# Kernel optimization log

Measured on AMD Instinct MI355X. Metric: run time of the kernel, lower is better.

Reference implementation:

```python
import jax, jax.numpy as jnp
import numpy as np

B, C, H, W = 4, 64, 128, 128
Q = 65536
OUT_SIZE = 256  # output image side -> cell = 2/OUT_SIZE
HIDDEN = 256
D_IN = C + 2 + 2  # feat + rel_coord + rel_cell


def setup_inputs() -> dict:
    key = jax.random.key(0)
    ks = jax.random.split(key, 8)
    feat = jax.random.normal(ks[0], (B, C, H, W), dtype=jnp.float32)
    coord = jax.random.uniform(ks[1], (B, Q, 2), dtype=jnp.float32, minval=-1.0, maxval=1.0)
    cell = jnp.full((B, Q, 2), 2.0 / OUT_SIZE, dtype=jnp.float32)

    def lin(k, din, dout):
        return jax.random.normal(k, (din, dout), dtype=jnp.float32) * (1.0 / np.sqrt(din))

    w0 = lin(ks[2], D_IN, HIDDEN)
    w1 = lin(ks[3], HIDDEN, HIDDEN)
    w2 = lin(ks[4], HIDDEN, HIDDEN)
    w3 = lin(ks[5], HIDDEN, HIDDEN)
    w4 = lin(ks[6], HIDDEN, 3)
    z = lambda d: jnp.zeros((d,), dtype=jnp.float32)
    return {"feat": feat, "coord": coord, "cell": cell,
            "w0": w0, "b0": z(HIDDEN), "w1": w1, "b1": z(HIDDEN),
            "w2": w2, "b2": z(HIDDEN), "w3": w3, "b3": z(HIDDEN),
            "w4": w4, "b4": z(3)}


def _liif(feat, coord, cell, ws, bs):
    b, c, h, w = feat.shape
    eps = 1e-6
    rx, ry = 1.0 / h, 1.0 / w  # 2/h/2, 2/w/2
    # local ensemble shifts, loop order vx outer, vy inner: (-1,-1),(-1,1),(1,-1),(1,1)
    shifts = jnp.array([[-rx, -ry], [-rx, ry], [rx, -ry], [rx, ry]], dtype=feat.dtype) + eps
    feat_flat = feat.reshape(b, c, h * w)
    cell_scale = jnp.array([h, w], dtype=feat.dtype)
    rel_cell = cell * cell_scale  # same for all branches

    def branch(shift):
        cshift = jnp.clip(coord + shift, -1.0 + eps, 1.0 - eps)
        # nearest grid_sample, align_corners=False: idx = floor((x+1)*size/2), clamped
        iy = jnp.clip(jnp.floor((cshift[..., 0] + 1.0) * (h * 0.5)), 0.0, h - 1.0).astype(jnp.int32)
        ix = jnp.clip(jnp.floor((cshift[..., 1] + 1.0) * (w * 0.5)), 0.0, w - 1.0).astype(jnp.int32)
        idx = iy * w + ix  # [B, Q]
        q_feat = jnp.take_along_axis(feat_flat, idx[:, None, :], axis=2)  # [B, C, Q]
        q_feat = q_feat.transpose(0, 2, 1)  # [B, Q, C]
        # feat_coord at the gathered pixel (make_coord values)
        qc0 = -1.0 + (2.0 * iy.astype(feat.dtype) + 1.0) / h
        qc1 = -1.0 + (2.0 * ix.astype(feat.dtype) + 1.0) / w
        rel0 = (coord[..., 0] - qc0) * h
        rel1 = (coord[..., 1] - qc1) * w
        inp = jnp.concatenate([q_feat, rel0[..., None], rel1[..., None], rel_cell], axis=-1)
        x = inp
        for wi, bi in zip(ws[:-1], bs[:-1]):
            x = jax.nn.relu(x @ wi + bi)
        pred = x @ ws[-1] + bs[-1]  # [B, Q, 3]
        area = jnp.abs(rel0 * rel1) + 1e-9  # [B, Q]
        return pred, area

    preds, areas = jax.vmap(branch)(shifts)  # [4,B,Q,3], [4,B,Q]
    tot = areas.sum(axis=0)
    # diagonal weight swap: 0<->3, 1<->2  == reverse
    wgt = areas[::-1] / tot
    return (preds * wgt[..., None]).sum(axis=0)  # [B, Q, 3]


def reference(feat, coord, cell, w0, b0, w1, b1, w2, b2, w3, b3, w4, b4):
    ws = [w0, w1, w2, w3, w4]
    bs = [b0, b1, b2, b3, b4]
    return _liif(feat, coord, cell, ws, bs)
```

## Files before the change

### kernel.cpp

```cpp
#include <hip/hip_runtime.h>
#include <cstdint>

typedef __bf16 bf16x8 __attribute__((ext_vector_type(8)));
typedef float f32x4 __attribute__((ext_vector_type(4)));
typedef float f32x16 __attribute__((ext_vector_type(16)));
typedef unsigned int u32x4 __attribute__((ext_vector_type(4)));
typedef unsigned int u32x2 __attribute__((ext_vector_type(2)));
typedef unsigned short u16;
typedef unsigned int u32;

#define HH 128
#define WW 128
#define CC 64
#define QQ 65536
#define BB 4

#define RS 264

#define L0_OFF 0
#define L1_OFF 20480
#define L2_OFF 86016
#define L3_OFF 151552
#define W4_OFF 217088
#define FEATT_BYTE_OFF 524288u

__global__ void pack_weights(const float* __restrict__ w0,
                             const float* __restrict__ w1,
                             const float* __restrict__ w2,
                             const float* __restrict__ w3,
                             const float* __restrict__ w4,
                             u16* __restrict__ ws_us) {
    int bid = blockIdx.x;
    int lane = threadIdx.x;
    int dst, kbase, n, Ksrc, Ncols;
    const float* w;
    if (bid < 424) {
        int tile, off;
        if (bid < 40)       { tile = bid;       off = L0_OFF; w = w0; Ksrc = 68;  }
        else if (bid < 168) { tile = bid - 40;  off = L1_OFF; w = w1; Ksrc = 256; }
        else if (bid < 296) { tile = bid - 168; off = L2_OFF; w = w2; Ksrc = 256; }
        else                { tile = bid - 296; off = L3_OFF; w = w3; Ksrc = 256; }
        int nt = tile & 7, ks = tile >> 3;
        n = nt * 32 + (lane & 31);
        kbase = ks * 16 + (lane >> 5) * 8;
        Ncols = 256;
        dst = off + tile * 512 + lane * 8;
    } else {
        int kt = bid - 424;
        n = lane & 15;
        kbase = kt * 32 + (lane >> 4) * 8;
        w = w4; Ksrc = 256; Ncols = 3;
        dst = W4_OFF + kt * 512 + lane * 8;
    }
    unsigned int d[4];
    for (int i = 0; i < 4; ++i) {
        unsigned int lo, hi;
        {
            int k = kbase + 2 * i;
            float x = (k < Ksrc && n < Ncols) ? w[k * Ncols + n] : 0.0f;
            __bf16 hb = (__bf16)x;
            lo = (unsigned int)__builtin_bit_cast(u16, hb);
        }
        {
            int k = kbase + 2 * i + 1;
            float x = (k < Ksrc && n < Ncols) ? w[k * Ncols + n] : 0.0f;
            __bf16 hb = (__bf16)x;
            hi = (unsigned int)__builtin_bit_cast(u16, hb);
        }
        d[i] = lo | (hi << 16);
    }
    u32x4 pk = { d[0], d[1], d[2], d[3] };
    *reinterpret_cast<u32x4*>(ws_us + dst) = pk;
}

__global__ void prep_featT(const float* __restrict__ feat, u16* __restrict__ featT) {
    __shared__ u16 tile[128 * 66];
    int bid = blockIdx.x;
    int b = bid >> 7, y = bid & 127;
    for (int idx = threadIdx.x; idx < CC * WW; idx += 256) {
        int c = idx >> 7, x = idx & 127;
        float v = feat[(((b * CC + c) * HH + y) * WW) + x];
        __bf16 hb = (__bf16)v;
        tile[x * 66 + c] = __builtin_bit_cast(u16, hb);
    }
    __syncthreads();
    for (int idx = threadIdx.x; idx < 2048; idx += 256) {
        int x = idx >> 4, c4 = (idx & 15) * 4;
        const u16* src = tile + x * 66 + c4;
        u32x2 d;
        d[0] = (unsigned int)src[0] | ((unsigned int)src[1] << 16);
        d[1] = (unsigned int)src[2] | ((unsigned int)src[3] << 16);
        *reinterpret_cast<u32x2*>(featT + ((b * HH + y) * WW + x) * CC + c4) = d;
    }
}

__device__ __forceinline__ void preload6(u32x4 w[6], const u32x4* __restrict__ b,
                                         int v, int kstr) {
    w[0] = b[v];
    w[1] = b[v + 64];
    w[2] = b[v + kstr];
    w[3] = b[v + kstr + 64];
    w[4] = b[v + 2 * kstr];
    w[5] = b[v + 2 * kstr + 64];
}

template <int NKS>
__device__ __forceinline__ void gemm32(const u16* __restrict__ src,
                                       u16* __restrict__ dst,
                                       const u32x4* __restrict__ wbase,
                                       const float* __restrict__ bias,
                                       int wave, int lane,
                                       const u32x4 wpre[6],
                                       u32x4 wnxt[6],
                                       const u32x4* __restrict__ wnb,
                                       int vnxt, int nkstr) {
    f32x16 acc[2][2] = {};
    const int l31 = lane & 31;
    const int hi = lane >> 5;
    const int voff = wave * 128 + lane;
    const u16* xb = src + l31 * RS + hi * 8;
    u16* db = dst + l31 * RS + wave * 64 + hi * 4;

    u32x4 wq[3][2];
    wq[0][0] = wpre[0]; wq[0][1] = wpre[1];
    wq[1][0] = wpre[2]; wq[1][1] = wpre[3];
    wq[2][0] = wpre[4]; wq[2][1] = wpre[5];

    bf16x8 xc[2][2];
    xc[0][0] = __builtin_bit_cast(bf16x8, *reinterpret_cast<const u32x4*>(xb));
    xc[0][1] = __builtin_bit_cast(bf16x8, *reinterpret_cast<const u32x4*>(xb + 32 * RS));
    xc[1][0] = __builtin_bit_cast(bf16x8, *reinterpret_cast<const u32x4*>(xb + 16));
    xc[1][1] = __builtin_bit_cast(bf16x8, *reinterpret_cast<const u32x4*>(xb + 32 * RS + 16));

#pragma unroll
    for (int ks = 0; ks < NKS; ++ks) {
        const int ws = ks % 3;
        const int xs = ks & 1;
        acc[0][0] = __builtin_amdgcn_mfma_f32_32x32x16_bf16(
            __builtin_bit_cast(bf16x8, wq[ws][0]), xc[xs][0], acc[0][0], 0, 0, 0);
        acc[1][0] = __builtin_amdgcn_mfma_f32_32x32x16_bf16(
            __builtin_bit_cast(bf16x8, wq[ws][1]), xc[xs][0], acc[1][0], 0, 0, 0);
        if (ks + 2 < NKS)
            xc[xs][0] = __builtin_bit_cast(bf16x8,
                *reinterpret_cast<const u32x4*>(xb + (ks + 2) * 16));
        acc[0][1] = __builtin_amdgcn_mfma_f32_32x32x16_bf16(
            __builtin_bit_cast(bf16x8, wq[ws][0]), xc[xs][1], acc[0][1], 0, 0, 0);
        acc[1][1] = __builtin_amdgcn_mfma_f32_32x32x16_bf16(
            __builtin_bit_cast(bf16x8, wq[ws][1]), xc[xs][1], acc[1][1], 0, 0, 0);
        if (ks + 2 < NKS)
            xc[xs][1] = __builtin_bit_cast(bf16x8,
                *reinterpret_cast<const u32x4*>(xb + 32 * RS + (ks + 2) * 16));
        if (ks + 3 < NKS) {
            const u32x4* wn = wbase + (ks + 3) * 512;
            wq[ws][0] = wn[voff];
            wq[ws][1] = wn[voff + 64];
        }
    }

    wnxt[0] = wnb[vnxt];
    wnxt[1] = wnb[vnxt + 64];
    wnxt[2] = wnb[vnxt + nkstr];
    wnxt[3] = wnb[vnxt + nkstr + 64];
    wnxt[4] = wnb[vnxt + 2 * nkstr];
    wnxt[5] = wnb[vnxt + 2 * nkstr + 64];

#pragma unroll
    for (int ft = 0; ft < 2; ++ft) {
        const int fb = wave * 64 + ft * 32 + hi * 4;
#pragma unroll
        for (int q4 = 0; q4 < 4; ++q4) {
            f32x4 bv = *reinterpret_cast<const f32x4*>(bias + fb + q4 * 8);
#pragma unroll
            for (int st = 0; st < 2; ++st) {
                float v0 = fmaxf(acc[ft][st][q4 * 4 + 0] + bv[0], 0.0f);
                float v1 = fmaxf(acc[ft][st][q4 * 4 + 1] + bv[1], 0.0f);
                float v2 = fmaxf(acc[ft][st][q4 * 4 + 2] + bv[2], 0.0f);
                float v3 = fmaxf(acc[ft][st][q4 * 4 + 3] + bv[3], 0.0f);
                __bf16 h0 = (__bf16)v0, h1 = (__bf16)v1, h2 = (__bf16)v2, h3 = (__bf16)v3;
                u32x2 d;
                d[0] = (u32)__builtin_bit_cast(u16, h0) | ((u32)__builtin_bit_cast(u16, h1) << 16);
                d[1] = (u32)__builtin_bit_cast(u16, h2) | ((u32)__builtin_bit_cast(u16, h3) << 16);
                *reinterpret_cast<u32x2*>(db + st * 32 * RS + ft * 32 + q4 * 8) = d;
            }
        }
    }
}

__global__ __launch_bounds__(256, 2) void liif_main(
    const float* __restrict__ coord, const float* __restrict__ cell,
    const float* __restrict__ b0, const float* __restrict__ b1,
    const float* __restrict__ b2, const float* __restrict__ b3,
    const float* __restrict__ b4,
    const u16* __restrict__ wpack, const u16* __restrict__ featT,
    float* __restrict__ out) {
    __shared__ u16 bufs[2 * 64 * RS];
    __shared__ float areasLDS[64];

    u16* buf0 = bufs;
    u16* buf1 = bufs + 64 * RS;

    const int t = threadIdx.x;
    const int wave = t >> 6, lane = t & 63;
    const int row = t >> 2, p = t & 3;

    const int bq = blockIdx.x * 16 + (row >> 2);
    const int v = row & 3;
    const int b = bq >> 16;
    const float c0 = coord[bq * 2 + 0];
    const float c1 = coord[bq * 2 + 1];
    const float rc0 = cell[bq * 2 + 0] * 128.0f;
    const float rc1 = cell[bq * 2 + 1] * 128.0f;
    const float eps = 1e-6f;
    const float sx = ((v & 2) ? 0.0078125f : -0.0078125f) + eps;
    const float sy = ((v & 1) ? 0.0078125f : -0.0078125f) + eps;
    float cs0 = fminf(fmaxf(c0 + sx, -1.0f + eps), 1.0f - eps);
    float cs1 = fminf(fmaxf(c1 + sy, -1.0f + eps), 1.0f - eps);
    float fy = fminf(fmaxf(floorf((cs0 + 1.0f) * 64.0f), 0.0f), 127.0f);
    float fx = fminf(fmaxf(floorf((cs1 + 1.0f) * 64.0f), 0.0f), 127.0f);
    int iy = (int)fy, ix = (int)fx;
    float qc0 = -1.0f + (2.0f * fy + 1.0f) * 0.0078125f;
    float qc1 = -1.0f + (2.0f * fx + 1.0f) * 0.0078125f;
    float rel0 = (c0 - qc0) * 128.0f;
    float rel1 = (c1 - qc1) * 128.0f;
    float area = fabsf(rel0 * rel1) + 1e-9f;

    {
        const u16* fr = featT + (((b * HH + iy) * WW + ix) * CC) + p * 16;
        u32x4 f0 = *reinterpret_cast<const u32x4*>(fr);
        u32x4 f1 = *reinterpret_cast<const u32x4*>(fr + 8);
        u16* sb = buf0 + row * RS;
        *reinterpret_cast<u32x4*>(sb + p * 16) = f0;
        *reinterpret_cast<u32x4*>(sb + p * 16 + 8) = f1;
        u32x4 e = { 0u, 0u, 0u, 0u };
        if (p == 0) {
            __bf16 h0 = (__bf16)rel0, h1 = (__bf16)rel1, h2 = (__bf16)rc0, h3 = (__bf16)rc1;
            e[0] = (u32)__builtin_bit_cast(u16, h0) | ((u32)__builtin_bit_cast(u16, h1) << 16);
            e[1] = (u32)__builtin_bit_cast(u16, h2) | ((u32)__builtin_bit_cast(u16, h3) << 16);
            areasLDS[row] = area;
        }
        *reinterpret_cast<u32x4*>(sb + 64 + p * 8) = e;
    }

    const u32x4* wp = reinterpret_cast<const u32x4*>(wpack);
    const u32x4* wp0 = wp + (L0_OFF / 8);
    const u32x4* wp1 = wp + (L1_OFF / 8);
    const u32x4* wp2 = wp + (L2_OFF / 8);
    const u32x4* wp3 = wp + (L3_OFF / 8);
    const u32x4* wp4 = wp + (W4_OFF / 8);
    const int voff = wave * 128 + lane;

    u32x4 wA[6], wB[6];
    preload6(wA, wp0, voff, 512);
    __syncthreads();
    gemm32<5>(buf0, buf1, wp0, b0, wave, lane, wA, wB, wp1, voff, 512);
    __syncthreads();
    gemm32<16>(buf1, buf0, wp1, b1, wave, lane, wB, wA, wp2, voff, 512);
    __syncthreads();
    gemm32<16>(buf0, buf1, wp2, b2, wave, lane, wA, wB, wp3, voff, 512);
    __syncthreads();
    gemm32<16>(buf1, buf0, wp3, b3, wave, lane, wB, wA, wp4, lane, 128);
    u32x4 w4hi[2];
#pragma unroll
    for (int kt = 0; kt < 2; ++kt) w4hi[kt] = wp4[(kt + 6) * 64 + lane];
    __syncthreads();

    const int l15 = lane & 15;
    const int qd = lane >> 4;
    const u16* xb = buf0 + (wave * 16 + l15) * RS + qd * 8;
    f32x4 accf = {};
#pragma unroll
    for (int kt = 0; kt < 6; ++kt) {
        bf16x8 x = __builtin_bit_cast(bf16x8,
            *reinterpret_cast<const u32x4*>(xb + kt * 32));
        accf = __builtin_amdgcn_mfma_f32_16x16x32_bf16(
            __builtin_bit_cast(bf16x8, wA[kt]), x, accf, 0, 0, 0);
    }
#pragma unroll
    for (int kt = 6; kt < 8; ++kt) {
        bf16x8 x = __builtin_bit_cast(bf16x8,
            *reinterpret_cast<const u32x4*>(xb + kt * 32));
        accf = __builtin_amdgcn_mfma_f32_16x16x32_bf16(
            __builtin_bit_cast(bf16x8, w4hi[kt - 6]), x, accf, 0, 0, 0);
    }
    float a = areasLDS[wave * 16 + l15];
    float a1 = a + __shfl_xor(a, 1);
    float asum = a1 + __shfl_xor(a1, 2);
    float aopp = __shfl_xor(a, 3);
    float wgt = aopp / asum;
    float o0 = (accf[0] + b4[0]) * wgt;
    float o1 = (accf[1] + b4[1]) * wgt;
    float o2 = (accf[2] + b4[2]) * wgt;
    o0 += __shfl_xor(o0, 1); o0 += __shfl_xor(o0, 2);
    o1 += __shfl_xor(o1, 1); o1 += __shfl_xor(o1, 2);
    o2 += __shfl_xor(o2, 1); o2 += __shfl_xor(o2, 2);

    if (qd == 0 && (l15 & 3) == 0) {
        int obq = blockIdx.x * 16 + wave * 4 + (l15 >> 2);
        out[obq * 3 + 0] = o0;
        out[obq * 3 + 1] = o1;
        out[obq * 3 + 2] = o2;
    }
}

extern "C" void kernel_launch(void* const* d_in, const int* in_sizes, int n_in,
                              void* d_out, int out_size, void* d_ws, size_t ws_size,
                              hipStream_t stream) {
    const float* feat  = (const float*)d_in[0];
    const float* coord = (const float*)d_in[1];
    const float* cell  = (const float*)d_in[2];
    const float* w0 = (const float*)d_in[3];
    const float* b0 = (const float*)d_in[4];
    const float* w1 = (const float*)d_in[5];
    const float* b1 = (const float*)d_in[6];
    const float* w2 = (const float*)d_in[7];
    const float* b2 = (const float*)d_in[8];
    const float* w3 = (const float*)d_in[9];
    const float* b3 = (const float*)d_in[10];
    const float* w4 = (const float*)d_in[11];
    const float* b4 = (const float*)d_in[12];

    u16* ws_us = (u16*)d_ws;
    u16* featT = (u16*)((char*)d_ws + FEATT_BYTE_OFF);

    hipLaunchKernelGGL(pack_weights, dim3(432), dim3(64), 0, stream,
                       w0, w1, w2, w3, w4, ws_us);
    hipLaunchKernelGGL(prep_featT, dim3(BB * HH), dim3(256), 0, stream, feat, featT);
    hipLaunchKernelGGL(liif_main, dim3((BB * QQ) / 16), dim3(256), 0, stream,
                       coord, cell, b0, b1, b2, b3, b4, ws_us, featT,
                       (float*)d_out);
}
```

Baseline: 579.0 us.

## Double rows per block and reuse weight fragments across four MFMA tiles

```diff
diff --git a/kernel.cpp b/kernel.cpp
--- a/kernel.cpp
+++ b/kernel.cpp
@@ -105,8 +105,7 @@
 }
 
 template <int NKS>
-__device__ __forceinline__ void gemm32(const u16* __restrict__ src,
-                                       u16* __restrict__ dst,
+__device__ __forceinline__ void gemm32(u16* buf,
                                        const u32x4* __restrict__ wbase,
                                        const float* __restrict__ bias,
                                        int wave, int lane,
@@ -114,42 +113,41 @@
                                        u32x4 wnxt[6],
                                        const u32x4* __restrict__ wnb,
                                        int vnxt, int nkstr) {
-    f32x16 acc[2][2] = {};
+    f32x16 acc[2][4] = {};
     const int l31 = lane & 31;
     const int hi = lane >> 5;
     const int voff = wave * 128 + lane;
-    const u16* xb = src + l31 * RS + hi * 8;
-    u16* db = dst + l31 * RS + wave * 64 + hi * 4;
+    const u16* xb = buf + l31 * RS + hi * 8;
+    u16* db = buf + l31 * RS + wave * 64 + hi * 4;
 
     u32x4 wq[3][2];
     wq[0][0] = wpre[0]; wq[0][1] = wpre[1];
     wq[1][0] = wpre[2]; wq[1][1] = wpre[3];
     wq[2][0] = wpre[4]; wq[2][1] = wpre[5];
 
-    bf16x8 xc[2][2];
-    xc[0][0] = __builtin_bit_cast(bf16x8, *reinterpret_cast<const u32x4*>(xb));
-    xc[0][1] = __builtin_bit_cast(bf16x8, *reinterpret_cast<const u32x4*>(xb + 32 * RS));
-    xc[1][0] = __builtin_bit_cast(bf16x8, *reinterpret_cast<const u32x4*>(xb + 16));
-    xc[1][1] = __builtin_bit_cast(bf16x8, *reinterpret_cast<const u32x4*>(xb + 32 * RS + 16));
+    bf16x8 xc[2][4];
+#pragma unroll
+    for (int st = 0; st < 4; ++st) {
+        xc[0][st] = __builtin_bit_cast(bf16x8,
+            *reinterpret_cast<const u32x4*>(xb + st * 32 * RS));
+        xc[1][st] = __builtin_bit_cast(bf16x8,
+            *reinterpret_cast<const u32x4*>(xb + st * 32 * RS + 16));
+    }
 
 #pragma unroll
     for (int ks = 0; ks < NKS; ++ks) {
         const int ws = ks % 3;
         const int xs = ks & 1;
-        acc[0][0] = __builtin_amdgcn_mfma_f32_32x32x16_bf16(
-            __builtin_bit_cast(bf16x8, wq[ws][0]), xc[xs][0], acc[0][0], 0, 0, 0);
-        acc[1][0] = __builtin_amdgcn_mfma_f32_32x32x16_bf16(
-            __builtin_bit_cast(bf16x8, wq[ws][1]), xc[xs][0], acc[1][0], 0, 0, 0);
-        if (ks + 2 < NKS)
-            xc[xs][0] = __builtin_bit_cast(bf16x8,
-                *reinterpret_cast<const u32x4*>(xb + (ks + 2) * 16));
-        acc[0][1] = __builtin_amdgcn_mfma_f32_32x32x16_bf16(
-            __builtin_bit_cast(bf16x8, wq[ws][0]), xc[xs][1], acc[0][1], 0, 0, 0);
-        acc[1][1] = __builtin_amdgcn_mfma_f32_32x32x16_bf16(
-            __builtin_bit_cast(bf16x8, wq[ws][1]), xc[xs][1], acc[1][1], 0, 0, 0);
-        if (ks + 2 < NKS)
-            xc[xs][1] = __builtin_bit_cast(bf16x8,
-                *reinterpret_cast<const u32x4*>(xb + 32 * RS + (ks + 2) * 16));
+#pragma unroll
+        for (int st = 0; st < 4; ++st) {
+            acc[0][st] = __builtin_amdgcn_mfma_f32_32x32x16_bf16(
+                __builtin_bit_cast(bf16x8, wq[ws][0]), xc[xs][st], acc[0][st], 0, 0, 0);
+            acc[1][st] = __builtin_amdgcn_mfma_f32_32x32x16_bf16(
+                __builtin_bit_cast(bf16x8, wq[ws][1]), xc[xs][st], acc[1][st], 0, 0, 0);
+            if (ks + 2 < NKS)
+                xc[xs][st] = __builtin_bit_cast(bf16x8,
+                    *reinterpret_cast<const u32x4*>(xb + st * 32 * RS + (ks + 2) * 16));
+        }
         if (ks + 3 < NKS) {
             const u32x4* wn = wbase + (ks + 3) * 512;
             wq[ws][0] = wn[voff];
@@ -164,6 +162,8 @@
     wnxt[4] = wnb[vnxt + 2 * nkstr];
     wnxt[5] = wnb[vnxt + 2 * nkstr + 64];
 
+    __syncthreads();
+
 #pragma unroll
     for (int ft = 0; ft < 2; ++ft) {
         const int fb = wave * 64 + ft * 32 + hi * 4;
@@ -171,7 +171,7 @@
         for (int q4 = 0; q4 < 4; ++q4) {
             f32x4 bv = *reinterpret_cast<const f32x4*>(bias + fb + q4 * 8);
 #pragma unroll
-            for (int st = 0; st < 2; ++st) {
+            for (int st = 0; st < 4; ++st) {
                 float v0 = fmaxf(acc[ft][st][q4 * 4 + 0] + bv[0], 0.0f);
                 float v1 = fmaxf(acc[ft][st][q4 * 4 + 1] + bv[1], 0.0f);
                 float v2 = fmaxf(acc[ft][st][q4 * 4 + 2] + bv[2], 0.0f);
@@ -193,17 +193,14 @@
     const float* __restrict__ b4,
     const u16* __restrict__ wpack, const u16* __restrict__ featT,
     float* __restrict__ out) {
-    __shared__ u16 bufs[2 * 64 * RS];
-    __shared__ float areasLDS[64];
-
-    u16* buf0 = bufs;
-    u16* buf1 = bufs + 64 * RS;
+    __shared__ u16 bufA[128 * RS];
+    __shared__ float areasLDS[128];
 
     const int t = threadIdx.x;
     const int wave = t >> 6, lane = t & 63;
-    const int row = t >> 2, p = t & 3;
-
-    const int bq = blockIdx.x * 16 + (row >> 2);
+    const int row = t >> 1, p = t & 1;
+
+    const int bq = blockIdx.x * 32 + (row >> 2);
     const int v = row & 3;
     const int b = bq >> 16;
     const float c0 = coord[bq * 2 + 0];
@@ -225,20 +222,26 @@
     float area = fabsf(rel0 * rel1) + 1e-9f;
 
     {
-        const u16* fr = featT + (((b * HH + iy) * WW + ix) * CC) + p * 16;
+        const u16* fr = featT + (((b * HH + iy) * WW + ix) * CC) + p * 32;
         u32x4 f0 = *reinterpret_cast<const u32x4*>(fr);
         u32x4 f1 = *reinterpret_cast<const u32x4*>(fr + 8);
-        u16* sb = buf0 + row * RS;
-        *reinterpret_cast<u32x4*>(sb + p * 16) = f0;
-        *reinterpret_cast<u32x4*>(sb + p * 16 + 8) = f1;
+        u32x4 f2 = *reinterpret_cast<const u32x4*>(fr + 16);
+        u32x4 f3 = *reinterpret_cast<const u32x4*>(fr + 24);
+        u16* sb = bufA + row * RS;
+        *reinterpret_cast<u32x4*>(sb + p * 32) = f0;
+        *reinterpret_cast<u32x4*>(sb + p * 32 + 8) = f1;
+        *reinterpret_cast<u32x4*>(sb + p * 32 + 16) = f2;
+        *reinterpret_cast<u32x4*>(sb + p * 32 + 24) = f3;
         u32x4 e = { 0u, 0u, 0u, 0u };
+        u32x4 z = { 0u, 0u, 0u, 0u };
         if (p == 0) {
             __bf16 h0 = (__bf16)rel0, h1 = (__bf16)rel1, h2 = (__bf16)rc0, h3 = (__bf16)rc1;
             e[0] = (u32)__builtin_bit_cast(u16, h0) | ((u32)__builtin_bit_cast(u16, h1) << 16);
             e[1] = (u32)__builtin_bit_cast(u16, h2) | ((u32)__builtin_bit_cast(u16, h3) << 16);
             areasLDS[row] = area;
         }
-        *reinterpret_cast<u32x4*>(sb + 64 + p * 8) = e;
+        *reinterpret_cast<u32x4*>(sb + 64 + p * 16) = e;
+        *reinterpret_cast<u32x4*>(sb + 64 + p * 16 + 8) = z;
     }
 
     const u32x4* wp = reinterpret_cast<const u32x4*>(wpack);
@@ -252,13 +255,13 @@
     u32x4 wA[6], wB[6];
     preload6(wA, wp0, voff, 512);
     __syncthreads();
-    gemm32<5>(buf0, buf1, wp0, b0, wave, lane, wA, wB, wp1, voff, 512);
-    __syncthreads();
-    gemm32<16>(buf1, buf0, wp1, b1, wave, lane, wB, wA, wp2, voff, 512);
-    __syncthreads();
-    gemm32<16>(buf0, buf1, wp2, b2, wave, lane, wA, wB, wp3, voff, 512);
-    __syncthreads();
-    gemm32<16>(buf1, buf0, wp3, b3, wave, lane, wB, wA, wp4, lane, 128);
+    gemm32<5>(bufA, wp0, b0, wave, lane, wA, wB, wp1, voff, 512);
+    __syncthreads();
+    gemm32<16>(bufA, wp1, b1, wave, lane, wB, wA, wp2, voff, 512);
+    __syncthreads();
+    gemm32<16>(bufA, wp2, b2, wave, lane, wA, wB, wp3, voff, 512);
+    __syncthreads();
+    gemm32<16>(bufA, wp3, b3, wave, lane, wB, wA, wp4, lane, 128);
     u32x4 w4hi[2];
 #pragma unroll
     for (int kt = 0; kt < 2; ++kt) w4hi[kt] = wp4[(kt + 6) * 64 + lane];
@@ -266,39 +269,37 @@
 
     const int l15 = lane & 15;
     const int qd = lane >> 4;
-    const u16* xb = buf0 + (wave * 16 + l15) * RS + qd * 8;
-    f32x4 accf = {};
-#pragma unroll
-    for (int kt = 0; kt < 6; ++kt) {
-        bf16x8 x = __builtin_bit_cast(bf16x8,
-            *reinterpret_cast<const u32x4*>(xb + kt * 32));
-        accf = __builtin_amdgcn_mfma_f32_16x16x32_bf16(
-            __builtin_bit_cast(bf16x8, wA[kt]), x, accf, 0, 0, 0);
-    }
-#pragma unroll
-    for (int kt = 6; kt < 8; ++kt) {
-        bf16x8 x = __builtin_bit_cast(bf16x8,
-            *reinterpret_cast<const u32x4*>(xb + kt * 32));
-        accf = __builtin_amdgcn_mfma_f32_16x16x32_bf16(
-            __builtin_bit_cast(bf16x8, w4hi[kt - 6]), x, accf, 0, 0, 0);
-    }
-    float a = areasLDS[wave * 16 + l15];
-    float a1 = a + __shfl_xor(a, 1);
-    float asum = a1 + __shfl_xor(a1, 2);
-    float aopp = __shfl_xor(a, 3);
-    float wgt = aopp / asum;
-    float o0 = (accf[0] + b4[0]) * wgt;
-    float o1 = (accf[1] + b4[1]) * wgt;
-    float o2 = (accf[2] + b4[2]) * wgt;
-    o0 += __shfl_xor(o0, 1); o0 += __shfl_xor(o0, 2);
-    o1 += __shfl_xor(o1, 1); o1 += __shfl_xor(o1, 2);
-    o2 += __shfl_xor(o2, 1); o2 += __shfl_xor(o2, 2);
-
-    if (qd == 0 && (l15 & 3) == 0) {
-        int obq = blockIdx.x * 16 + wave * 4 + (l15 >> 2);
-        out[obq * 3 + 0] = o0;
-        out[obq * 3 + 1] = o1;
-        out[obq * 3 + 2] = o2;
+    const u16* xb4 = bufA + (wave * 32 + l15) * RS + qd * 8;
+    f32x4 accf[2] = {};
+#pragma unroll
+    for (int kt = 0; kt < 8; ++kt) {
+        bf16x8 a = __builtin_bit_cast(bf16x8, (kt < 6) ? wA[kt] : w4hi[kt - 6]);
+        bf16x8 x0 = __builtin_bit_cast(bf16x8,
+            *reinterpret_cast<const u32x4*>(xb4 + kt * 32));
+        accf[0] = __builtin_amdgcn_mfma_f32_16x16x32_bf16(a, x0, accf[0], 0, 0, 0);
+        bf16x8 x1 = __builtin_bit_cast(bf16x8,
+            *reinterpret_cast<const u32x4*>(xb4 + 16 * RS + kt * 32));
+        accf[1] = __builtin_amdgcn_mfma_f32_16x16x32_bf16(a, x1, accf[1], 0, 0, 0);
+    }
+#pragma unroll
+    for (int stl = 0; stl < 2; ++stl) {
+        float a = areasLDS[wave * 32 + stl * 16 + l15];
+        float a1 = a + __shfl_xor(a, 1);
+        float asum = a1 + __shfl_xor(a1, 2);
+        float aopp = __shfl_xor(a, 3);
+        float wgt = aopp / asum;
+        float o0 = (accf[stl][0] + b4[0]) * wgt;
+        float o1 = (accf[stl][1] + b4[1]) * wgt;
+        float o2 = (accf[stl][2] + b4[2]) * wgt;
+        o0 += __shfl_xor(o0, 1); o0 += __shfl_xor(o0, 2);
+        o1 += __shfl_xor(o1, 1); o1 += __shfl_xor(o1, 2);
+        o2 += __shfl_xor(o2, 1); o2 += __shfl_xor(o2, 2);
+        if (qd == 0 && (l15 & 3) == 0) {
+            int obq = blockIdx.x * 32 + wave * 8 + stl * 4 + (l15 >> 2);
+            out[obq * 3 + 0] = o0;
+            out[obq * 3 + 1] = o1;
+            out[obq * 3 + 2] = o2;
+        }
     }
 }
 
@@ -325,7 +326,7 @@
     hipLaunchKernelGGL(pack_weights, dim3(432), dim3(64), 0, stream,
                        w0, w1, w2, w3, w4, ws_us);
     hipLaunchKernelGGL(prep_featT, dim3(BB * HH), dim3(256), 0, stream, feat, featT);
-    hipLaunchKernelGGL(liif_main, dim3((BB * QQ) / 16), dim3(256), 0, stream,
+    hipLaunchKernelGGL(liif_main, dim3((BB * QQ) / 32), dim3(256), 0, stream,
                        coord, cell, b0, b1, b2, b3, b4, ws_us, featT,
                        (float*)d_out);
 }
```

New measurement: 502.0 us. 13.3% less time.
